# Performance work log

Measured on AMD Instinct MI355X. Metric: run time of the kernel, lower is better.

Reference implementation:

```python
import jax, jax.numpy as jnp
import numpy as np

N_PATCHES = 131072
N_BAGS = 128
IN_DIM = 1024
HID_DIM = 512
OUT_DIM = 2


def setup_inputs() -> dict:
    key = jax.random.key(0)
    k1, k2, k3, k4 = jax.random.split(key, 4)
    features = jax.random.normal(k1, (N_PATCHES, IN_DIM), dtype=jnp.float32)
    attention = jax.random.uniform(k2, (N_PATCHES, 2), dtype=jnp.float32)
    bag_sizes = jnp.full((N_BAGS,), N_PATCHES // N_BAGS, dtype=jnp.int32)
    # MLP params (Linear 1024->512, ReLU, Linear 512->2)
    W1 = jax.random.normal(k3, (IN_DIM, HID_DIM), dtype=jnp.float32) / np.sqrt(IN_DIM)
    b1 = jnp.zeros((HID_DIM,), dtype=jnp.float32)
    W2 = jax.random.normal(k4, (HID_DIM, OUT_DIM), dtype=jnp.float32) / np.sqrt(HID_DIM)
    b2 = jnp.zeros((OUT_DIM,), dtype=jnp.float32)
    return {"features": features, "attention": attention, "bag_sizes": bag_sizes,
            "W1": W1, "b1": b1, "W2": W2, "b2": b2}


def reference(features, attention, bag_sizes, W1, b1, W2, b2):
    # MLP: Linear -> ReLU -> Linear
    h = jax.nn.relu(features @ W1 + b1)            # [N, HID]
    raw_logits = h @ W2 + b2                       # [N, OUT]
    pos_att = attention[:, 0:1]                    # [N, 1]
    neg_att = attention[:, 1:2]                    # [N, 1]
    pos_evidence = pos_att * jax.nn.relu(raw_logits)
    neg_evidence = neg_att * jax.nn.relu(-raw_logits)
    net_evidence = pos_evidence - neg_evidence     # [N, OUT]
    # ragged per-bag segment sum (bags are contiguous runs of patches)
    seg_ids = jnp.repeat(jnp.arange(N_BAGS), bag_sizes, total_repeat_length=N_PATCHES)
    bag_logits = jax.ops.segment_sum(net_evidence, seg_ids, num_segments=N_BAGS)  # [B, OUT]
    return bag_logits, pos_evidence, neg_evidence, net_evidence
```

## Files before the change

kernel.cpp:

```cpp
#include <hip/hip_runtime.h>

constexpr int NP  = 131072;
constexpr int NB  = 128;
constexpr int IND = 1024;
constexpr int HID = 512;
constexpr int BK  = 64;

typedef __bf16 bf16x8 __attribute__((ext_vector_type(8)));
typedef float  f32x4  __attribute__((ext_vector_type(4)));

typedef __attribute__((address_space(1))) const unsigned int gu32;
typedef __attribute__((address_space(3))) unsigned int       lu32;

__device__ __forceinline__ unsigned short f2bf(float f) {
    unsigned int u = __float_as_uint(f);
    u += 0x7fff + ((u >> 16) & 1);
    return (unsigned short)(u >> 16);
}

__global__ __launch_bounds__(256) void k_w1t(const float* __restrict__ W1,
                                             unsigned short* __restrict__ W1T) {
    __shared__ float tile[32][33];
    const int kt = blockIdx.x;
    const int nt = blockIdx.y;
    const int tx = threadIdx.x & 31;
    const int ty = threadIdx.x >> 5;
#pragma unroll
    for (int i = 0; i < 4; ++i)
        tile[ty + i * 8][tx] = W1[(kt * 32 + ty + i * 8) * HID + nt * 32 + tx];
    __syncthreads();
#pragma unroll
    for (int i = 0; i < 4; ++i)
        W1T[(size_t)(nt * 32 + ty + i * 8) * IND + kt * 32 + tx] = f2bf(tile[tx][ty + i * 8]);
}

__global__ __launch_bounds__(512, 4) void k_fused(
    const float* __restrict__ feat, const float* __restrict__ att,
    const unsigned short* __restrict__ W1T,
    const float* __restrict__ b1, const float* __restrict__ W2,
    const float* __restrict__ b2,
    float* __restrict__ out_bag, float* __restrict__ out_pos,
    float* __restrict__ out_neg, float* __restrict__ out_net)
{
    __shared__ __align__(16) union {
        struct { unsigned short A[64 * BK]; unsigned short B[HID * BK]; } g;
        struct { float part[8][64][2]; float netsm[64][2]; } e;
    } sm;

    const int tid  = threadIdx.x;
    const int w    = tid >> 6;
    const int lane = tid & 63;
    const int quad = lane >> 4;
    const int n16  = lane & 15;
    const int row0 = blockIdx.x * 64;

    f32x4 acc[4][4];
#pragma unroll
    for (int mt = 0; mt < 4; ++mt)
#pragma unroll
        for (int t = 0; t < 4; ++t)
#pragma unroll
            for (int e = 0; e < 4; ++e) acc[mt][t][e] = 0.f;

    const int ar = tid >> 3;
    const int as = tid & 7;
    const float* aptr = feat + (size_t)(row0 + ar) * IND + as * 8;
    unsigned short* a_dst = &sm.g.A[ar * BK + (as ^ (ar & 7)) * 8];

    const int bn   = tid >> 3;
    const int bls  = (tid & 7) ^ (bn & 7);
    const unsigned short* bsrc = W1T + (size_t)bn * IND + bls * 8;
    unsigned short* b_dst = &sm.g.B[bn * BK + (tid & 7) * 8];

    float4 av0 = *reinterpret_cast<const float4*>(aptr);
    float4 av1 = *reinterpret_cast<const float4*>(aptr + 4);

    for (int k0 = 0; k0 < IND; k0 += BK) {
#pragma unroll
        for (int j = 0; j < 8; ++j)
            __builtin_amdgcn_global_load_lds(
                (gu32*)(bsrc + (size_t)j * 64 * IND + k0),
                (lu32*)(b_dst + j * 64 * BK),
                16, 0, 0);

        unsigned short ab[8] = { f2bf(av0.x), f2bf(av0.y), f2bf(av0.z), f2bf(av0.w),
                                 f2bf(av1.x), f2bf(av1.y), f2bf(av1.z), f2bf(av1.w) };
        *reinterpret_cast<uint4*>(a_dst) = *reinterpret_cast<const uint4*>(ab);

        if (k0 + BK < IND) {
            av0 = *reinterpret_cast<const float4*>(aptr + k0 + BK);
            av1 = *reinterpret_cast<const float4*>(aptr + k0 + BK + 4);
        }
        __syncthreads();

#pragma unroll
        for (int kk = 0; kk < 2; ++kk) {
            const int ps = ((kk * 4 + quad) ^ (n16 & 7)) * 8;
            bf16x8 afr[4], bfr[4];
#pragma unroll
            for (int mt = 0; mt < 4; ++mt)
                afr[mt] = *reinterpret_cast<const bf16x8*>(&sm.g.A[(mt * 16 + n16) * BK + ps]);
#pragma unroll
            for (int t = 0; t < 4; ++t)
                bfr[t] = *reinterpret_cast<const bf16x8*>(&sm.g.B[(w * 64 + t * 16 + n16) * BK + ps]);
#pragma unroll
            for (int mt = 0; mt < 4; ++mt)
#pragma unroll
                for (int t = 0; t < 4; ++t)
                    acc[mt][t] = __builtin_amdgcn_mfma_f32_16x16x32_bf16(afr[mt], bfr[t], acc[mt][t], 0, 0, 0);
        }
        __syncthreads();
    }

    float lp[16][2];
#pragma unroll
    for (int i = 0; i < 16; ++i) { lp[i][0] = 0.f; lp[i][1] = 0.f; }
#pragma unroll
    for (int t = 0; t < 4; ++t) {
        int col = (w * 4 + t) * 16 + n16;
        float bias = b1[col];
        float w20 = W2[col * 2], w21 = W2[col * 2 + 1];
#pragma unroll
        for (int mt = 0; mt < 4; ++mt)
#pragma unroll
            for (int r = 0; r < 4; ++r) {
                float h = fmaxf(acc[mt][t][r] + bias, 0.f);
                lp[mt * 4 + r][0] += h * w20;
                lp[mt * 4 + r][1] += h * w21;
            }
    }
#pragma unroll
    for (int off = 8; off >= 1; off >>= 1)
#pragma unroll
        for (int i = 0; i < 16; ++i) {
            lp[i][0] += __shfl_xor(lp[i][0], off);
            lp[i][1] += __shfl_xor(lp[i][1], off);
        }
    if (n16 == 0) {
#pragma unroll
        for (int mt = 0; mt < 4; ++mt)
#pragma unroll
            for (int r = 0; r < 4; ++r) {
                sm.e.part[w][mt * 16 + quad * 4 + r][0] = lp[mt * 4 + r][0];
                sm.e.part[w][mt * 16 + quad * 4 + r][1] = lp[mt * 4 + r][1];
            }
    }
    __syncthreads();

    if (tid < 128) {
        int r = tid >> 1, j = tid & 1;
        float raw = b2[j];
#pragma unroll
        for (int ww = 0; ww < 8; ++ww) raw += sm.e.part[ww][r][j];
        int grow = row0 + r;
        float a0 = att[grow * 2], a1 = att[grow * 2 + 1];
        float pos = a0 * fmaxf(raw, 0.f);
        float neg = a1 * fmaxf(-raw, 0.f);
        float net = pos - neg;
        out_pos[grow * 2 + j] = pos;
        out_neg[grow * 2 + j] = neg;
        out_net[grow * 2 + j] = net;
        sm.e.netsm[r][j] = net;
    }
    __syncthreads();

    if (tid < 2) {
        float s = 0.f;
#pragma unroll 8
        for (int r = 0; r < 64; ++r) s += sm.e.netsm[r][tid];
        atomicAdd(&out_bag[(row0 >> 10) * 2 + tid], s);
    }
}

extern "C" void kernel_launch(void* const* d_in, const int* in_sizes, int n_in,
                              void* d_out, int out_size, void* d_ws, size_t ws_size,
                              hipStream_t stream) {
    const float* feat = (const float*)d_in[0];
    const float* att  = (const float*)d_in[1];
    const float* W1   = (const float*)d_in[3];
    const float* b1   = (const float*)d_in[4];
    const float* W2   = (const float*)d_in[5];
    const float* b2   = (const float*)d_in[6];
    float* out = (float*)d_out;
    unsigned short* W1T = (unsigned short*)d_ws;

    hipMemsetAsync(out, 0, NB * 2 * sizeof(float), stream);
    k_w1t<<<dim3(32, 16), 256, 0, stream>>>(W1, W1T);
    k_fused<<<NP / 64, 512, 0, stream>>>(feat, att, W1T, b1, W2, b2,
                                         out,
                                         out + 256,
                                         out + 256 + NP * 2,
                                         out + 256 + NP * 4);
}
```

Baseline: 754.1 us.

## Double-buffer LDS tiles with halved K-step and one barrier per iteration

Cuts the K tile from 64 to 32 and double-buffers the A and B LDS tiles, so the next tile's W1 async-to-LDS loads and the bf16 feature conversion overlap the MFMAs on the current tile. Each iteration now needs one barrier instead of two. Total LDS size stays the same. The XOR swizzle on the LDS layout is dropped, which risks bank conflicts on the 16-byte fragment reads, and the loop runs twice as many iterations, each with less work to hide latency behind.

```diff
diff --git a/kernel.cpp b/kernel.cpp
--- a/kernel.cpp
+++ b/kernel.cpp
@@ -4,7 +4,8 @@
 constexpr int NB  = 128;
 constexpr int IND = 1024;
 constexpr int HID = 512;
-constexpr int BK  = 64;
+constexpr int BK  = 32;
+constexpr int NIT = IND / BK;
 
 typedef __bf16 bf16x8 __attribute__((ext_vector_type(8)));
 typedef float  f32x4  __attribute__((ext_vector_type(4)));
@@ -43,7 +44,7 @@
     float* __restrict__ out_neg, float* __restrict__ out_net)
 {
     __shared__ __align__(16) union {
-        struct { unsigned short A[64 * BK]; unsigned short B[HID * BK]; } g;
+        struct { unsigned short A[2][64 * BK]; unsigned short B[2][HID * BK]; } g;
         struct { float part[8][64][2]; float netsm[64][2]; } e;
     } sm;
 
@@ -62,53 +63,51 @@
 #pragma unroll
             for (int e = 0; e < 4; ++e) acc[mt][t][e] = 0.f;
 
-    const int ar = tid >> 3;
-    const int as = tid & 7;
-    const float* aptr = feat + (size_t)(row0 + ar) * IND + as * 8;
-    unsigned short* a_dst = &sm.g.A[ar * BK + (as ^ (ar & 7)) * 8];
+    const int ar = tid >> 3, as = tid & 7;
+    const float* aptr = feat + (size_t)(row0 + ar) * IND + as * 4;
+    const int a_off = ar * BK + as * 4;
 
-    const int bn   = tid >> 3;
-    const int bls  = (tid & 7) ^ (bn & 7);
-    const unsigned short* bsrc = W1T + (size_t)bn * IND + bls * 8;
-    unsigned short* b_dst = &sm.g.B[bn * BK + (tid & 7) * 8];
+    const int bn = tid >> 2, bs = tid & 3;
+    const unsigned short* bsrc = W1T + (size_t)bn * IND + bs * 8;
+    const int b_off = bn * BK + bs * 8;
 
-    float4 av0 = *reinterpret_cast<const float4*>(aptr);
-    float4 av1 = *reinterpret_cast<const float4*>(aptr + 4);
-
-    for (int k0 = 0; k0 < IND; k0 += BK) {
+    float4 av = *reinterpret_cast<const float4*>(aptr);
 #pragma unroll
-        for (int j = 0; j < 8; ++j)
-            __builtin_amdgcn_global_load_lds(
-                (gu32*)(bsrc + (size_t)j * 64 * IND + k0),
-                (lu32*)(b_dst + j * 64 * BK),
-                16, 0, 0);
-
-        unsigned short ab[8] = { f2bf(av0.x), f2bf(av0.y), f2bf(av0.z), f2bf(av0.w),
-                                 f2bf(av1.x), f2bf(av1.y), f2bf(av1.z), f2bf(av1.w) };
-        *reinterpret_cast<uint4*>(a_dst) = *reinterpret_cast<const uint4*>(ab);
-
-        if (k0 + BK < IND) {
-            av0 = *reinterpret_cast<const float4*>(aptr + k0 + BK);
-            av1 = *reinterpret_cast<const float4*>(aptr + k0 + BK + 4);
-        }
-        __syncthreads();
+    for (int j = 0; j < 4; ++j)
+        __builtin_amdgcn_global_load_lds((gu32*)(bsrc + (size_t)j * 128 * IND),
+                                         (lu32*)(&sm.g.B[0][j * 128 * BK + b_off]), 16, 0, 0);
+    {
+        unsigned short ab[4] = { f2bf(av.x), f2bf(av.y), f2bf(av.z), f2bf(av.w) };
+        *reinterpret_cast<ushort4*>(&sm.g.A[0][a_off]) = *reinterpret_cast<const ushort4*>(ab);
+    }
+    av = *reinterpret_cast<const float4*>(aptr + BK);
+    __syncthreads();
 
 #pragma unroll
-        for (int kk = 0; kk < 2; ++kk) {
-            const int ps = ((kk * 4 + quad) ^ (n16 & 7)) * 8;
-            bf16x8 afr[4], bfr[4];
+    for (int i = 0; i < NIT; ++i) {
+        const int cur = i & 1, nxt = cur ^ 1;
+        if (i < NIT - 1) {
 #pragma unroll
-            for (int mt = 0; mt < 4; ++mt)
-                afr[mt] = *reinterpret_cast<const bf16x8*>(&sm.g.A[(mt * 16 + n16) * BK + ps]);
+            for (int j = 0; j < 4; ++j)
+                __builtin_amdgcn_global_load_lds(
+                    (gu32*)(bsrc + (size_t)j * 128 * IND + (i + 1) * BK),
+                    (lu32*)(&sm.g.B[nxt][j * 128 * BK + b_off]), 16, 0, 0);
+            unsigned short ab[4] = { f2bf(av.x), f2bf(av.y), f2bf(av.z), f2bf(av.w) };
+            *reinterpret_cast<ushort4*>(&sm.g.A[nxt][a_off]) = *reinterpret_cast<const ushort4*>(ab);
+            if (i < NIT - 2) av = *reinterpret_cast<const float4*>(aptr + (i + 2) * BK);
+        }
+        bf16x8 afr[4], bfr[4];
+#pragma unroll
+        for (int mt = 0; mt < 4; ++mt)
+            afr[mt] = *reinterpret_cast<const bf16x8*>(&sm.g.A[cur][(mt * 16 + n16) * BK + quad * 8]);
+#pragma unroll
+        for (int t = 0; t < 4; ++t)
+            bfr[t] = *reinterpret_cast<const bf16x8*>(&sm.g.B[cur][(w * 64 + t * 16 + n16) * BK + quad * 8]);
+#pragma unroll
+        for (int mt = 0; mt < 4; ++mt)
 #pragma unroll
             for (int t = 0; t < 4; ++t)
-                bfr[t] = *reinterpret_cast<const bf16x8*>(&sm.g.B[(w * 64 + t * 16 + n16) * BK + ps]);
-#pragma unroll
-            for (int mt = 0; mt < 4; ++mt)
-#pragma unroll
-                for (int t = 0; t < 4; ++t)
-                    acc[mt][t] = __builtin_amdgcn_mfma_f32_16x16x32_bf16(afr[mt], bfr[t], acc[mt][t], 0, 0, 0);
-        }
+                acc[mt][t] = __builtin_amdgcn_mfma_f32_16x16x32_bf16(afr[mt], bfr[t], acc[mt][t], 0, 0, 0);
         __syncthreads();
     }
 
```

New measurement: 816.2 us. 8.2% more time.
